# Kernel optimization log

Hardware: AMD Instinct MI355X
Metric: run time of the kernel (lower is better)

## Reference

```python
import jax, jax.numpy as jnp
import numpy as np

B, T, I, H, O = 128, 64, 512, 1024, 512
EPS = 0.01
N_MAX = 12  # static max ACT ponder steps per timestep (halts at ~2 steps at init)


def setup_inputs() -> dict:
    key = jax.random.key(0)
    ks = jax.random.split(key, 10)
    k = 1.0 / np.sqrt(H)
    u = lambda kk, shape: jax.random.uniform(kk, shape, jnp.float32, -k, k)
    return {
        "x": jax.random.normal(ks[0], (B, T, I), jnp.float32),
        "s0": jax.random.normal(ks[1], (1, B, H), jnp.float32) * 0.1,
        "w_ih": u(ks[2], (H, 1 + I)),
        "w_hh": u(ks[3], (H, H)),
        "b_ih": u(ks[4], (H,)),
        "b_hh": u(ks[5], (H,)),
        "w_halt": u(ks[6], (1, H)),
        "b_halt": u(ks[7], (1,)),
        "w_out": u(ks[8], (O, H)),
        "b_out": u(ks[9], (O,)),
    }


def _binarize_st(p):
    # Binarize autograd.Function: forward -> 1 where p > 0 (sigmoid outputs are
    # always positive, zeroed halted entries stay 0); backward -> identity (STE).
    return p + jax.lax.stop_gradient(jnp.where(p > 0, 1.0, 0.0) - p)


def reference(x, s0, w_ih, w_hh, b_ih, b_hh, w_halt, b_halt, w_out, b_out):
    def cell(inp, h):  # inp [B,1+I], h [B,H] -> tanh RNN cell
        return jnp.tanh(inp @ w_ih.T + b_ih + h @ w_hh.T + b_hh)

    def timestep(h_carry, x_t):  # h_carry [B,H], x_t [B,I]
        ones = jnp.ones((B, 1), x_t.dtype)
        x1 = jnp.concatenate([ones, x_t], axis=1)          # flag=1: first ponder step
        x0 = jnp.concatenate([ones * 0.0, x_t], axis=1)    # flag=0: continued pondering
        # ponder step 0 (always contributes for every sample)
        h = cell(x1, h_carry)
        out = h @ w_out.T + b_out                 # [B,O]
        p = jax.nn.sigmoid(h @ w_halt.T + b_halt) # [B,1]
        w = _binarize_st(p)
        out_acc = out * w
        h_acc = h * w
        cum = p[:, 0]
        # ponder value is only assigned when a sample halts at step 0 (original bug kept)
        pond = jnp.where(cum >= 1.0 - EPS, 2.0, 0.0)

        def ponder_step(carry, _):
            h_prev, cum, out_acc, h_acc = carry
            active = (cum < 1.0 - EPS).astype(h_prev.dtype)[:, None]  # [B,1]
            h = cell(x0, h_prev) * active
            out = (h @ w_out.T + b_out) * active
            p = jax.nn.sigmoid(h @ w_halt.T + b_halt) * active
            w = _binarize_st(p)
            return (h, cum + p[:, 0], out_acc + out * w, h_acc + h * w), None

        (h, cum, out_acc, h_acc), _ = jax.lax.scan(
            ponder_step, (h, cum, out_acc, h_acc), None, length=N_MAX - 1)
        # next-timestep hidden is the binarized-weight accumulation of states
        return h_acc, (out_acc, pond)

    h_last, (outputs, ponder) = jax.lax.scan(timestep, s0[0], jnp.swapaxes(x, 0, 1))
    return jnp.swapaxes(outputs, 0, 1), jnp.swapaxes(ponder, 0, 1)  # [B,T,O], [B,T]
```

## Files before the change

### kernel.cpp

```cpp
#include <hip/hip_runtime.h>
#include <hip/hip_cooperative_groups.h>
#include <math.h>

namespace cg = cooperative_groups;

#define NB 128
#define NT 64
#define NI 512
#define NH 1024
#define NO 512
#define PONDOFF (NB*NT*NO)

extern __shared__ float smem[];

__device__ __forceinline__ void group_barrier(unsigned* ctr, unsigned target, int tid)
{
    __syncthreads();
    if (tid == 0) {
        __hip_atomic_fetch_add(ctr, 1u, __ATOMIC_RELEASE, __HIP_MEMORY_SCOPE_AGENT);
        while (__hip_atomic_fetch_add(ctr, 0u, __ATOMIC_RELAXED,
                                      __HIP_MEMORY_SCOPE_AGENT) < target)
            __builtin_amdgcn_s_sleep(1);
    }
    if (tid < 64)
        __builtin_amdgcn_fence(__ATOMIC_ACQUIRE, "agent");
    __syncthreads();
}

__global__ void __launch_bounds__(1024, 1)
arnn_coop(const float* __restrict__ x, const float* __restrict__ s0,
          const float* __restrict__ w_ih, const float* __restrict__ w_hh,
          const float* __restrict__ b_ih, const float* __restrict__ b_hh,
          const float* __restrict__ w_halt, const float* __restrict__ b_halt,
          const float* __restrict__ w_out, const float* __restrict__ b_out,
          float* __restrict__ out, float* __restrict__ ws)
{
    cg::grid_group grid = cg::this_grid();
    const int tid = threadIdx.x;
    const int bid = blockIdx.x;
    const int gid = bid * 1024 + tid;

    float* wihT  = ws;
    float* hbuf  = wihT + NI*NH;
    float* habuf = hbuf + NB*2*NH;
    unsigned* ctrA = (unsigned*)(habuf + 2*NB*NH);

    const int gp = bid >> 5, lb = bid & 31;

    __shared__ float s_whalt[NH];
    __shared__ int   s_t[16];
    __shared__ float s_cum[16];
    __shared__ int   s_n[16];
    __shared__ int   s_et[16], s_en[16];
    __shared__ unsigned char s_sl[16];
    __shared__ unsigned char s_run[16];
    __shared__ unsigned char s_mode[16];
    __shared__ unsigned char s_epi[16];
    __shared__ int s_alive;

    for (int e = gid; e < NI*NH; e += 256*1024) {
        const int i = e >> 10, jj = e & 1023;
        wihT[e] = w_ih[jj*(NI+1) + 1 + i];
    }
    if (gid < 8*16)
        __hip_atomic_store(&ctrA[gid], 0u, __ATOMIC_RELAXED, __HIP_MEMORY_SCOPE_AGENT);
    for (int e = tid; e < 1024*32; e += 1024) {
        const int k = e & 1023, jj = e >> 10;
        const float v = w_hh[(lb*32 + jj)*NH + k];
        const int su = (jj >> 1) ^ ((k >> 6) & 15);
        smem[k*32 + su*2 + (jj & 1)] = v;
    }
    s_whalt[tid & 1023] = w_halt[tid & 1023];
    if (tid < 16) {
        s_t[tid] = 0; s_cum[tid] = 0.0f; s_n[tid] = 0;
        s_et[tid] = 0; s_en[tid] = 0;
        s_sl[tid] = 0; s_run[tid] = 1; s_mode[tid] = 0; s_epi[tid] = 0;
    }
    if (tid == 0) s_alive = 1;
    grid.sync();

    unsigned* ctr = ctrA + gp*16;

    const int w    = tid >> 6;
    const int lane = tid & 63;
    const int rq   = w >> 2;
    const int co   = w & 3;
    const int up   = lane & 3;
    const int ks   = lane >> 2;
    const int u    = co*4 + up;
    const int jg   = lb*32 + u*2;
    const int b0   = gp*16 + rq*4;
    const bool k0  = (ks == 0);
    const int ldsb = ks*2048 + ((u ^ ks) << 1);

    const float bh  = b_halt[0];
    const float bias0 = k0 ? (b_ih[jg]   + b_hh[jg])   : 0.0f;
    const float bias1 = k0 ? (b_ih[jg+1] + b_hh[jg+1]) : 0.0f;
    const float w0a   = k0 ? w_ih[jg*(NI+1)]     : 0.0f;
    const float w0b   = k0 ? w_ih[(jg+1)*(NI+1)] : 0.0f;

    const int   eo = lb*16 + (lane & 15);
    const int   eq = lane >> 4;
    const int   eb = gp*16 + w;
    const float bo = b_out[eo];

    auto decide_p = [&](int slot) -> float {
        const float* hr = hbuf + ((gp*16 + w)*2 + slot)*NH + lane*16;
        float d = 0.0f;
        #pragma unroll
        for (int q = 0; q < 16; q += 4) {
            const float4 hv = *(const float4*)(hr + q);
            const float4 wv = *(const float4*)(&s_whalt[lane*16 + q]);
            d += hv.x*wv.x + hv.y*wv.y + hv.z*wv.z + hv.w*wv.w;
        }
        d += __shfl_xor(d, 1);  d += __shfl_xor(d, 2);  d += __shfl_xor(d, 4);
        d += __shfl_xor(d, 8);  d += __shfl_xor(d, 16); d += __shfl_xor(d, 32);
        return 1.0f / (1.0f + expf(-(d + bh)));
    };

    float xw[4][2];

    unsigned gen = 0;
    for (;;) {
        if (s_epi[w]) {
            const int et = s_et[w];
            const float* ha = habuf + (et&1)*(NB*NH) + eb*NH + eq*256;
            const float* wq = w_out + eo*NH + eq*256;
            float acc = 0.0f;
            #pragma unroll 4
            for (int jj2 = 0; jj2 < 256; jj2 += 4) {
                const float4 hv = *(const float4*)(ha + jj2);
                const float4 wv = *(const float4*)(wq + jj2);
                acc += hv.x*wv.x + hv.y*wv.y + hv.z*wv.z + hv.w*wv.w;
            }
            acc += __shfl_xor(acc, 16); acc += __shfl_xor(acc, 32);
            if (eq == 0) out[(eb*NT + et)*NO + eo] = acc + (float)s_en[w]*bo;
        }
        int ex[4], md[4], tt[4], sl[4];
        #pragma unroll
        for (int r = 0; r < 4; ++r) {
            const int rr = rq*4 + r;
            ex[r] = s_run[rr]; md[r] = s_mode[rr]; tt[r] = s_t[rr]; sl[r] = s_sl[rr];
        }
        if (ex[0] | ex[1] | ex[2] | ex[3]) {
            #pragma unroll
            for (int r = 0; r < 4; ++r) {
                if (ex[r] && md[r] == 0) {
                    float o0 = bias0, o1 = bias1;
                    const float* xr = x + ((b0+r)*NT + tt[r])*NI + ks*32;
                    const float* wp = wihT + (ks*32)*NH + jg;
                    #pragma unroll 4
                    for (int i = 0; i < 32; i += 4) {
                        const float4 xv = *(const float4*)(xr + i);
                        const float2 wa = *(const float2*)(wp + (i  )*NH);
                        const float2 wb = *(const float2*)(wp + (i+1)*NH);
                        const float2 wc = *(const float2*)(wp + (i+2)*NH);
                        const float2 wd = *(const float2*)(wp + (i+3)*NH);
                        o0 += xv.x*wa.x + xv.y*wb.x + xv.z*wc.x + xv.w*wd.x;
                        o1 += xv.x*wa.y + xv.y*wb.y + xv.z*wc.y + xv.w*wd.y;
                    }
                    xw[r][0] = o0; xw[r][1] = o1;
                }
            }
            float a[4][2];
            const float* hp[4];
            #pragma unroll
            for (int r = 0; r < 4; ++r) {
                const int b = b0 + r;
                a[r][0] = xw[r][0] + (md[r] == 0 ? w0a : 0.0f);
                a[r][1] = xw[r][1] + (md[r] == 0 ? w0b : 0.0f);
                if (!ex[r])           hp[r] = hbuf + (b*2)*NH + ks*64;
                else if (md[r] == 0)  hp[r] = (tt[r] == 0 ? s0 + b*NH
                                              : habuf + ((tt[r]-1)&1)*(NB*NH) + b*NH) + ks*64;
                else                  hp[r] = hbuf + (b*2 + sl[r])*NH + ks*64;
            }
            #pragma unroll 4
            for (int kc = 0; kc < 64; kc += 4) {
                const float4 h0 = *(const float4*)(hp[0] + kc);
                const float4 h1 = *(const float4*)(hp[1] + kc);
                const float4 h2 = *(const float4*)(hp[2] + kc);
                const float4 h3 = *(const float4*)(hp[3] + kc);
                const float2 wa = *(const float2*)(smem + ldsb + (kc  )*32);
                const float2 wb = *(const float2*)(smem + ldsb + (kc+1)*32);
                const float2 wc = *(const float2*)(smem + ldsb + (kc+2)*32);
                const float2 wd = *(const float2*)(smem + ldsb + (kc+3)*32);
                a[0][0] += h0.x*wa.x + h0.y*wb.x + h0.z*wc.x + h0.w*wd.x;
                a[0][1] += h0.x*wa.y + h0.y*wb.y + h0.z*wc.y + h0.w*wd.y;
                a[1][0] += h1.x*wa.x + h1.y*wb.x + h1.z*wc.x + h1.w*wd.x;
                a[1][1] += h1.x*wa.y + h1.y*wb.y + h1.z*wc.y + h1.w*wd.y;
                a[2][0] += h2.x*wa.x + h2.y*wb.x + h2.z*wc.x + h2.w*wd.x;
                a[2][1] += h2.x*wa.y + h2.y*wb.y + h2.z*wc.y + h2.w*wd.y;
                a[3][0] += h3.x*wa.x + h3.y*wb.x + h3.z*wc.x + h3.w*wd.x;
                a[3][1] += h3.x*wa.y + h3.y*wb.y + h3.z*wc.y + h3.w*wd.y;
            }
            #pragma unroll
            for (int r = 0; r < 4; ++r)
                #pragma unroll
                for (int c = 0; c < 2; ++c) {
                    float v = a[r][c];
                    v += __shfl_xor(v, 4);  v += __shfl_xor(v, 8);
                    v += __shfl_xor(v, 16); v += __shfl_xor(v, 32);
                    a[r][c] = v;
                }
            if (k0) {
                #pragma unroll
                for (int r = 0; r < 4; ++r) {
                    if (ex[r]) {
                        const float ha = tanhf(a[r][0]), hb = tanhf(a[r][1]);
                        const int b = b0 + r;
                        float* hw = hbuf + (b*2 + (sl[r]^1))*NH + jg;
                        hw[0] = ha; hw[1] = hb;
                        float* hq = habuf + (tt[r]&1)*(NB*NH) + b*NH + jg;
                        if (md[r] == 0) { hq[0] = ha;  hq[1] = hb;  }
                        else            { hq[0] += ha; hq[1] += hb; }
                    }
                }
            }
        }
        ++gen; group_barrier(ctr, 32*gen, tid);
        const int exw = s_run[w];
        float p = 0.0f;
        if (exw) p = decide_p(s_sl[w] ^ 1);
        if (lane == 0) {
            int newepi = 0;
            if (exw) {
                const int t = s_t[w];
                float cum; int n;
                if (s_mode[w] == 0) {
                    cum = p; n = 1;
                    if (lb == 0) out[PONDOFF + (gp*16 + w)*NT + t] = (p >= 0.99f) ? 2.0f : 0.0f;
                } else {
                    cum = s_cum[w] + p; n = s_n[w] + 1;
                }
                s_cum[w] = cum; s_n[w] = n;
                s_sl[w] ^= 1;
                if ((cum < 0.99f) && n < 12) {
                    s_mode[w] = 1;
                } else {
                    newepi = 1; s_et[w] = t; s_en[w] = n;
                    if (t == NT-1) s_run[w] = 0;
                    else { s_t[w] = t + 1; s_mode[w] = 0; }
                }
            }
            s_epi[w] = newepi;
        }
        __syncthreads();
        if (w == 0) {
            const int al = (lane < 16) ? (s_run[lane] | s_epi[lane]) : 0;
            const unsigned long long m = __ballot(al);
            if (lane == 0) s_alive = (m != 0ULL) ? 1 : 0;
        }
        __syncthreads();
        if (!s_alive) break;
    }
}

extern "C" void kernel_launch(void* const* d_in, const int* in_sizes, int n_in,
                              void* d_out, int out_size, void* d_ws, size_t ws_size,
                              hipStream_t stream) {
    const float* x      = (const float*)d_in[0];
    const float* s0     = (const float*)d_in[1];
    const float* w_ih   = (const float*)d_in[2];
    const float* w_hh   = (const float*)d_in[3];
    const float* b_ih   = (const float*)d_in[4];
    const float* b_hh   = (const float*)d_in[5];
    const float* w_halt = (const float*)d_in[6];
    const float* b_halt = (const float*)d_in[7];
    const float* w_out  = (const float*)d_in[8];
    const float* b_out  = (const float*)d_in[9];
    float* out = (float*)d_out;
    float* ws  = (float*)d_ws;

    static const int kLds = 131072;
    hipFuncSetAttribute((const void*)arnn_coop,
                        hipFuncAttributeMaxDynamicSharedMemorySize, kLds);

    void* args[] = { (void*)&x, (void*)&s0, (void*)&w_ih, (void*)&w_hh,
                     (void*)&b_ih, (void*)&b_hh, (void*)&w_halt, (void*)&b_halt,
                     (void*)&w_out, (void*)&b_out, (void*)&out, (void*)&ws };
    hipLaunchCooperativeKernel((void*)arnn_coop, dim3(256), dim3(1024), args, kLds, stream);
}
```

Measured before the change: 9.440 ms.

## Replace acquire fences with coherent atomic loads and keep h accumulator in registers

Shared cross-block buffers are now read and written through relaxed agent-scope atomic loads and stores, so the per-barrier acquire fence can be dropped and the spin loop uses a plain atomic load with a longer sleep. The habuf accumulation is kept in registers instead of a read-modify-write on global memory. Other changes: the halt-weight LDS array is padded to avoid bank conflicts, the per-group counter stride is widened, and the loop-exit vote is done per wave, which removes one __syncthreads. The risks are that splitting float4 loads into 64-bit atomics costs extra instructions, and that correctness now depends on relaxed atomics bypassing stale caches without a fence.

After: 12.32 ms. +30.5%, slower.

```diff
diff --git a/kernel.cpp b/kernel.cpp
--- a/kernel.cpp
+++ b/kernel.cpp
@@ -13,17 +13,31 @@
 
 extern __shared__ float smem[];
 
+typedef unsigned long long u64;
+
+__device__ __forceinline__ float2 ldcg2(const float* p) {
+    union { u64 u; float2 f; } c;
+    c.u = __hip_atomic_load((const u64*)p, __ATOMIC_RELAXED, __HIP_MEMORY_SCOPE_AGENT);
+    return c.f;
+}
+__device__ __forceinline__ void stcg2(float* p, float a, float b) {
+    union { u64 u; float2 f; } c;
+    c.f = make_float2(a, b);
+    __hip_atomic_store((u64*)p, c.u, __ATOMIC_RELAXED, __HIP_MEMORY_SCOPE_AGENT);
+}
+__device__ __forceinline__ void stcg1(float* p, float v) {
+    union { unsigned u; float f; } c; c.f = v;
+    __hip_atomic_store((unsigned*)p, c.u, __ATOMIC_RELAXED, __HIP_MEMORY_SCOPE_AGENT);
+}
+
 __device__ __forceinline__ void group_barrier(unsigned* ctr, unsigned target, int tid)
 {
     __syncthreads();
     if (tid == 0) {
         __hip_atomic_fetch_add(ctr, 1u, __ATOMIC_RELEASE, __HIP_MEMORY_SCOPE_AGENT);
-        while (__hip_atomic_fetch_add(ctr, 0u, __ATOMIC_RELAXED,
-                                      __HIP_MEMORY_SCOPE_AGENT) < target)
-            __builtin_amdgcn_s_sleep(1);
-    }
-    if (tid < 64)
-        __builtin_amdgcn_fence(__ATOMIC_ACQUIRE, "agent");
+        while (__hip_atomic_load(ctr, __ATOMIC_RELAXED, __HIP_MEMORY_SCOPE_AGENT) < target)
+            __builtin_amdgcn_s_sleep(2);
+    }
     __syncthreads();
 }
 
@@ -47,7 +61,7 @@
 
     const int gp = bid >> 5, lb = bid & 31;
 
-    __shared__ float s_whalt[NH];
+    __shared__ float s_whalt[NH + (NH/16)*4];
     __shared__ int   s_t[16];
     __shared__ float s_cum[16];
     __shared__ int   s_n[16];
@@ -56,13 +70,12 @@
     __shared__ unsigned char s_run[16];
     __shared__ unsigned char s_mode[16];
     __shared__ unsigned char s_epi[16];
-    __shared__ int s_alive;
 
     for (int e = gid; e < NI*NH; e += 256*1024) {
         const int i = e >> 10, jj = e & 1023;
         wihT[e] = w_ih[jj*(NI+1) + 1 + i];
     }
-    if (gid < 8*16)
+    if (gid < 8*32)
         __hip_atomic_store(&ctrA[gid], 0u, __ATOMIC_RELAXED, __HIP_MEMORY_SCOPE_AGENT);
     for (int e = tid; e < 1024*32; e += 1024) {
         const int k = e & 1023, jj = e >> 10;
@@ -70,16 +83,18 @@
         const int su = (jj >> 1) ^ ((k >> 6) & 15);
         smem[k*32 + su*2 + (jj & 1)] = v;
     }
-    s_whalt[tid & 1023] = w_halt[tid & 1023];
+    {
+        const int j = tid;
+        s_whalt[j + ((j >> 4) << 2)] = w_halt[j];
+    }
     if (tid < 16) {
         s_t[tid] = 0; s_cum[tid] = 0.0f; s_n[tid] = 0;
         s_et[tid] = 0; s_en[tid] = 0;
         s_sl[tid] = 0; s_run[tid] = 1; s_mode[tid] = 0; s_epi[tid] = 0;
     }
-    if (tid == 0) s_alive = 1;
     grid.sync();
 
-    unsigned* ctr = ctrA + gp*16;
+    unsigned* ctr = ctrA + gp*32;
 
     const int w    = tid >> 6;
     const int lane = tid & 63;
@@ -109,9 +124,10 @@
         float d = 0.0f;
         #pragma unroll
         for (int q = 0; q < 16; q += 4) {
-            const float4 hv = *(const float4*)(hr + q);
-            const float4 wv = *(const float4*)(&s_whalt[lane*16 + q]);
-            d += hv.x*wv.x + hv.y*wv.y + hv.z*wv.z + hv.w*wv.w;
+            const float2 h1 = ldcg2(hr + q);
+            const float2 h2 = ldcg2(hr + q + 2);
+            const float4 wv = *(const float4*)(&s_whalt[lane*20 + q]);
+            d += h1.x*wv.x + h1.y*wv.y + h2.x*wv.z + h2.y*wv.w;
         }
         d += __shfl_xor(d, 1);  d += __shfl_xor(d, 2);  d += __shfl_xor(d, 4);
         d += __shfl_xor(d, 8);  d += __shfl_xor(d, 16); d += __shfl_xor(d, 32);
@@ -119,22 +135,24 @@
     };
 
     float xw[4][2];
+    float hacc[4][2];
 
     unsigned gen = 0;
     for (;;) {
         if (s_epi[w]) {
             const int et = s_et[w];
-            const float* ha = habuf + (et&1)*(NB*NH) + eb*NH + eq*256;
+            const float* hap = habuf + (et&1)*(NB*NH) + eb*NH + eq*256;
             const float* wq = w_out + eo*NH + eq*256;
             float acc = 0.0f;
             #pragma unroll 4
             for (int jj2 = 0; jj2 < 256; jj2 += 4) {
-                const float4 hv = *(const float4*)(ha + jj2);
+                const float2 h1 = ldcg2(hap + jj2);
+                const float2 h2 = ldcg2(hap + jj2 + 2);
                 const float4 wv = *(const float4*)(wq + jj2);
-                acc += hv.x*wv.x + hv.y*wv.y + hv.z*wv.z + hv.w*wv.w;
+                acc += h1.x*wv.x + h1.y*wv.y + h2.x*wv.z + h2.y*wv.w;
             }
             acc += __shfl_xor(acc, 16); acc += __shfl_xor(acc, 32);
-            if (eq == 0) out[(eb*NT + et)*NO + eo] = acc + (float)s_en[w]*bo;
+            if (eq == 0) stcg1(&out[(eb*NT + et)*NO + eo], acc + (float)s_en[w]*bo);
         }
         int ex[4], md[4], tt[4], sl[4];
         #pragma unroll
@@ -176,22 +194,22 @@
             }
             #pragma unroll 4
             for (int kc = 0; kc < 64; kc += 4) {
-                const float4 h0 = *(const float4*)(hp[0] + kc);
-                const float4 h1 = *(const float4*)(hp[1] + kc);
-                const float4 h2 = *(const float4*)(hp[2] + kc);
-                const float4 h3 = *(const float4*)(hp[3] + kc);
+                const float2 h0a = ldcg2(hp[0] + kc), h0b = ldcg2(hp[0] + kc + 2);
+                const float2 h1a = ldcg2(hp[1] + kc), h1b = ldcg2(hp[1] + kc + 2);
+                const float2 h2a = ldcg2(hp[2] + kc), h2b = ldcg2(hp[2] + kc + 2);
+                const float2 h3a = ldcg2(hp[3] + kc), h3b = ldcg2(hp[3] + kc + 2);
                 const float2 wa = *(const float2*)(smem + ldsb + (kc  )*32);
                 const float2 wb = *(const float2*)(smem + ldsb + (kc+1)*32);
                 const float2 wc = *(const float2*)(smem + ldsb + (kc+2)*32);
                 const float2 wd = *(const float2*)(smem + ldsb + (kc+3)*32);
-                a[0][0] += h0.x*wa.x + h0.y*wb.x + h0.z*wc.x + h0.w*wd.x;
-                a[0][1] += h0.x*wa.y + h0.y*wb.y + h0.z*wc.y + h0.w*wd.y;
-                a[1][0] += h1.x*wa.x + h1.y*wb.x + h1.z*wc.x + h1.w*wd.x;
-                a[1][1] += h1.x*wa.y + h1.y*wb.y + h1.z*wc.y + h1.w*wd.y;
-                a[2][0] += h2.x*wa.x + h2.y*wb.x + h2.z*wc.x + h2.w*wd.x;
-                a[2][1] += h2.x*wa.y + h2.y*wb.y + h2.z*wc.y + h2.w*wd.y;
-                a[3][0] += h3.x*wa.x + h3.y*wb.x + h3.z*wc.x + h3.w*wd.x;
-                a[3][1] += h3.x*wa.y + h3.y*wb.y + h3.z*wc.y + h3.w*wd.y;
+                a[0][0] += h0a.x*wa.x + h0a.y*wb.x + h0b.x*wc.x + h0b.y*wd.x;
+                a[0][1] += h0a.x*wa.y + h0a.y*wb.y + h0b.x*wc.y + h0b.y*wd.y;
+                a[1][0] += h1a.x*wa.x + h1a.y*wb.x + h1b.x*wc.x + h1b.y*wd.x;
+                a[1][1] += h1a.x*wa.y + h1a.y*wb.y + h1b.x*wc.y + h1b.y*wd.y;
+                a[2][0] += h2a.x*wa.x + h2a.y*wb.x + h2b.x*wc.x + h2b.y*wd.x;
+                a[2][1] += h2a.x*wa.y + h2a.y*wb.y + h2b.x*wc.y + h2b.y*wd.y;
+                a[3][0] += h3a.x*wa.x + h3a.y*wb.x + h3b.x*wc.x + h3b.y*wd.x;
+                a[3][1] += h3a.x*wa.y + h3a.y*wb.y + h3b.x*wc.y + h3b.y*wd.y;
             }
             #pragma unroll
             for (int r = 0; r < 4; ++r)
@@ -208,11 +226,11 @@
                     if (ex[r]) {
                         const float ha = tanhf(a[r][0]), hb = tanhf(a[r][1]);
                         const int b = b0 + r;
-                        float* hw = hbuf + (b*2 + (sl[r]^1))*NH + jg;
-                        hw[0] = ha; hw[1] = hb;
-                        float* hq = habuf + (tt[r]&1)*(NB*NH) + b*NH + jg;
-                        if (md[r] == 0) { hq[0] = ha;  hq[1] = hb;  }
-                        else            { hq[0] += ha; hq[1] += hb; }
+                        stcg2(hbuf + (b*2 + (sl[r]^1))*NH + jg, ha, hb);
+                        if (md[r] == 0) { hacc[r][0] = ha;  hacc[r][1] = hb; }
+                        else            { hacc[r][0] += ha; hacc[r][1] += hb; }
+                        stcg2(habuf + (tt[r]&1)*(NB*NH) + b*NH + jg,
+                              hacc[r][0], hacc[r][1]);
                     }
                 }
             }
@@ -228,7 +246,9 @@
                 float cum; int n;
                 if (s_mode[w] == 0) {
                     cum = p; n = 1;
-                    if (lb == 0) out[PONDOFF + (gp*16 + w)*NT + t] = (p >= 0.99f) ? 2.0f : 0.0f;
+                    if (lb == 0)
+                        stcg1(&out[PONDOFF + (gp*16 + w)*NT + t],
+                              (p >= 0.99f) ? 2.0f : 0.0f);
                 } else {
                     cum = s_cum[w] + p; n = s_n[w] + 1;
                 }
@@ -245,13 +265,8 @@
             s_epi[w] = newepi;
         }
         __syncthreads();
-        if (w == 0) {
-            const int al = (lane < 16) ? (s_run[lane] | s_epi[lane]) : 0;
-            const unsigned long long m = __ballot(al);
-            if (lane == 0) s_alive = (m != 0ULL) ? 1 : 0;
-        }
-        __syncthreads();
-        if (!s_alive) break;
+        const int al = (lane < 16) ? (s_run[lane] | s_epi[lane]) : 0;
+        if (__ballot(al) == 0ULL) break;
     }
 }
 
```
